# Performance work log

Hardware: AMD Instinct MI355X
Metric: run time of the kernel (lower is better)

The kernel has to match this reference:

```python
import jax, jax.numpy as jnp
import numpy as np

B, N, DIM = 32, 1024, 768
H, S, D = 16, 4, 64  # num_heads, num_subheads (L=H*S=64), attn_dim


def setup_inputs() -> dict:
    key = jax.random.key(0)
    k1, k2, k3, k4 = jax.random.split(key, 4)
    x = jax.random.normal(k1, (B, N, DIM), dtype=jnp.float32)
    eos_indices = jax.random.randint(k2, (B,), 0, N)
    # q_emb: original shape (1,H,S,1,D); singleton dims dropped -> (H,S,D)
    q_emb = jax.random.normal(k3, (H, S, D), dtype=jnp.float32)
    # k Linear(dim -> H*D), xavier-uniform weight, zero bias (share_kv: v == k)
    limit = float(np.sqrt(6.0 / (DIM + H * D)))
    Wk = jax.random.uniform(k4, (DIM, H * D), dtype=jnp.float32, minval=-limit, maxval=limit)
    bk = jnp.zeros((H * D,), dtype=jnp.float32)
    return {"x": x, "eos_indices": eos_indices, "q_emb": q_emb, "Wk": Wk, "bk": bk}


def reference(x, eos_indices, q_emb, Wk, bk):
    # x: (B,N,dim); shared k/v projection -> (B,N,H,D)
    kv = (x @ Wk + bk).reshape(x.shape[0], x.shape[1], H, D)
    scale = D ** -0.5
    # Avoid the torch expand over subheads: contract directly.
    # logits: (B,H,S,N)
    logits = jnp.einsum("hsd,bnhd->bhsn", q_emb * scale, kv)
    # eos masking: positions strictly after eos index are masked out
    mask = jnp.arange(x.shape[1])[None, None, None, :] > eos_indices[:, None, None, None]
    logits = jnp.where(mask, -jnp.inf, logits)
    attn = jax.nn.softmax(logits, axis=-1)
    # weighted sum over N -> (B,H,S,D) -> (B,L,D)
    out = jnp.einsum("bhsn,bnhd->bhsd", attn, kv)
    return out.reshape(x.shape[0], H * S, D)
```

## Files before the change

kernel.cpp:

```cpp
#include <hip/hip_runtime.h>
#include <hip/hip_bf16.h>
#include <stdint.h>

typedef float  f32x4  __attribute__((ext_vector_type(4)));
typedef __bf16 bf16x4 __attribute__((ext_vector_type(4)));
typedef __bf16 bf16x8 __attribute__((ext_vector_type(8)));
typedef unsigned int u32x2 __attribute__((ext_vector_type(2)));
typedef unsigned int u32x4 __attribute__((ext_vector_type(4)));

#define AS1 __attribute__((address_space(1)))
#define AS3 __attribute__((address_space(3)))

__device__ __forceinline__ void async_load16(const void* g, void* lds) {
    __builtin_amdgcn_global_load_lds((const AS1 unsigned int*)g,
                                     (AS3 unsigned int*)lds, 16, 0, 0);
}

__global__ __launch_bounds__(256) void bias_init(const float* __restrict__ bk,
                                                 float* __restrict__ out) {
    const int idx = blockIdx.x * 256 + threadIdx.x;
    out[idx] = bk[((idx >> 8) & 15) * 64 + (idx & 63)];
}

__global__ __launch_bounds__(256) void qw_kernel(const float* __restrict__ q_emb,
                                                 const float* __restrict__ wk,
                                                 __bf16* __restrict__ qwT) {
    __shared__ float qlds[256];
    __shared__ float part[4096];
    const int t = threadIdx.x;
    const int kc = blockIdx.x;
    const int h  = blockIdx.y;
    const int k0 = kc * 64;
    qlds[t] = q_emb[h * 256 + t] * 0.125f;
    __syncthreads();
    const int dseg = t & 15;
    const int krow = t >> 4;
#pragma unroll
    for (int i = 0; i < 4; ++i) {
        const int k = i * 16 + krow;
        f32x4 wv = *(const f32x4*)&wk[(size_t)(k0 + k) * 1024 + h * 64 + dseg * 4];
#pragma unroll
        for (int s = 0; s < 4; ++s) {
            float p = qlds[s * 64 + dseg * 4 + 0] * wv[0]
                    + qlds[s * 64 + dseg * 4 + 1] * wv[1]
                    + qlds[s * 64 + dseg * 4 + 2] * wv[2]
                    + qlds[s * 64 + dseg * 4 + 3] * wv[3];
            part[k * 64 + s * 16 + dseg] = p;
        }
    }
    __syncthreads();
    const int k = t >> 2, s = t & 3;
    const float* pp = &part[k * 64 + s * 16];
    float sum = 0.f;
#pragma unroll
    for (int j = 0; j < 16; ++j) sum += pp[j];
    qwT[(h * 4 + s) * 768 + k0 + k] = (__bf16)sum;
}

__global__ __launch_bounds__(512) void logits_kernel(const float* __restrict__ x,
                                                     const __bf16* __restrict__ qwT,
                                                     const int* __restrict__ eos_idx,
                                                     __bf16* __restrict__ Lg,
                                                     float* __restrict__ partials) {
    __shared__ char smem[49152];
    char* Bl = smem;
    char* Al = smem + 16384;
    const int t = threadIdx.x, l = t & 63, w = t >> 6;
    const int m0 = blockIdx.x * 128;
    const int bb = m0 >> 10, n0 = m0 & 1023;
    const int chunk = blockIdx.x & 7;
    const int wrA = (w >> 1) * 32;
    const int wcB = (w & 1) * 32;

    f32x4 acc[2][2];
#pragma unroll
    for (int i = 0; i < 2; ++i)
#pragma unroll
        for (int j = 0; j < 2; ++j) acc[i][j] = (f32x4)0.f;

    const int Bcol = t >> 3, Bseg = t & 7;
    const __bf16* qsrc = qwT + Bcol * 768 + (Bseg ^ (Bcol & 7)) * 8;
    const int Arow0 = t >> 4;
    const int Aseg = t & 15;

    f32x4 av[4];
    async_load16(qsrc, Bl + t * 16);
#pragma unroll
    for (int i = 0; i < 4; ++i)
        av[i] = *(const f32x4*)&x[(size_t)(m0 + i * 32 + Arow0) * 768 + Aseg * 4];
#pragma unroll
    for (int i = 0; i < 4; ++i) {
        const int row = i * 32 + Arow0;
        bf16x4 vv = {(__bf16)av[i][0], (__bf16)av[i][1], (__bf16)av[i][2], (__bf16)av[i][3]};
        *(bf16x4*)(Al + ((row * 128 + Aseg * 8) ^ ((row & 7) << 4))) = vv;
    }
    asm volatile("s_waitcnt vmcnt(0)" ::: "memory");
    __syncthreads();

    int buf = 0;
    for (int step = 0; step < 12; ++step) {
        const int nbuf = buf ^ 1;
        const bool more = (step + 1) < 12;
        if (more) {
            const int kt = (step + 1) * 64;
            async_load16(qsrc + kt, Bl + nbuf * 8192 + t * 16);
#pragma unroll
            for (int i = 0; i < 4; ++i)
                av[i] = *(const f32x4*)&x[(size_t)(m0 + i * 32 + Arow0) * 768 + kt + Aseg * 4];
        }
#pragma unroll
        for (int kh = 0; kh < 2; ++kh) {
            const int u = kh * 4 + (l >> 4);
            bf16x8 af[2], bfr[2];
#pragma unroll
            for (int i = 0; i < 2; ++i) {
                const int row = wrA + i * 16 + (l & 15);
                af[i] = *(const bf16x8*)(Al + buf * 16384 +
                                         ((row * 128 + u * 16) ^ ((row & 7) << 4)));
            }
#pragma unroll
            for (int j = 0; j < 2; ++j) {
                const int col = wcB + j * 16 + (l & 15);
                bfr[j] = *(const bf16x8*)(Bl + buf * 8192 +
                                          ((col * 128 + u * 16) ^ ((col & 7) << 4)));
            }
#pragma unroll
            for (int i = 0; i < 2; ++i)
#pragma unroll
                for (int j = 0; j < 2; ++j)
                    acc[i][j] = __builtin_amdgcn_mfma_f32_16x16x32_bf16(
                        af[i], bfr[j], acc[i][j], 0, 0, 0);
        }
        if (more) {
#pragma unroll
            for (int i = 0; i < 4; ++i) {
                const int row = i * 32 + Arow0;
                bf16x4 vv = {(__bf16)av[i][0], (__bf16)av[i][1], (__bf16)av[i][2], (__bf16)av[i][3]};
                *(bf16x4*)(Al + nbuf * 16384 + ((row * 128 + Aseg * 8) ^ ((row & 7) << 4))) = vv;
            }
        }
        asm volatile("s_waitcnt vmcnt(0)" ::: "memory");
        __syncthreads();
        buf = nbuf;
    }

#pragma unroll
    for (int i = 0; i < 2; ++i)
#pragma unroll
        for (int j = 0; j < 2; ++j) {
            const int hs = wcB + j * 16 + (l & 15);
            const int nb = wrA + i * 16 + (l >> 4) * 4;
            *(f32x4*)(smem + ((hs * 512 + nb * 4) ^ ((hs & 7) << 4))) = acc[i][j];
        }
    __syncthreads();
    const int eosb = eos_idx[bb];
    const int hs = t >> 3, seg7 = t & 7;
    const int fH = (hs & 7) << 4;
    float mx = -INFINITY;
    bf16x4 pk4[4];
#pragma unroll
    for (int i = 0; i < 4; ++i) {
        const int seg = seg7 + i * 8;
        f32x4 v = *(const f32x4*)(smem + ((hs * 512 + seg * 16) ^ fH));
        bf16x4 pk;
#pragma unroll
        for (int j = 0; j < 4; ++j) {
            const float f = (n0 + seg * 4 + j > eosb) ? -INFINITY : v[j];
            pk[j] = (__bf16)f;
            mx = fmaxf(mx, (float)pk[j]);
        }
        pk4[i] = pk;
        *(bf16x4*)&Lg[(size_t)bb * 65536 + hs * 1024 + n0 + seg * 4] = pk;
    }
#pragma unroll
    for (int off = 1; off < 8; off <<= 1) mx = fmaxf(mx, __shfl_xor(mx, off));
    float sl = 0.f;
    if (mx > -INFINITY) {
#pragma unroll
        for (int i = 0; i < 4; ++i)
#pragma unroll
            for (int j = 0; j < 4; ++j) sl += __expf((float)pk4[i][j] - mx);
    }
#pragma unroll
    for (int off = 1; off < 8; off <<= 1) sl += __shfl_xor(sl, off);
    if (seg7 == 0) {
        float2 st = {mx, sl};
        *(float2*)&partials[(size_t)(((bb * 8 + chunk) * 64) + hs) * 2] = st;
    }
}

__global__ __launch_bounds__(256, 3) void pv_kernel(const float* __restrict__ x,
                                                    const __bf16* __restrict__ Lg,
                                                    const float* __restrict__ partials,
                                                    const float* __restrict__ wk,
                                                    float* __restrict__ out_p) {
    __shared__ char smem[32768];
    char* Pl = smem;
    char* Xl = smem + 16384;
    const int t = threadIdx.x, l = t & 63, w = t >> 6;
    const int vid = (blockIdx.x & 7) * 48 + (blockIdx.x >> 3);
    const int b = vid / 12, kc = vid % 12;
    const int k0 = kc * 64;
    const int wrA = (w >> 1) * 32, wcB = (w & 1) * 32;
    const __bf16* Lgb = Lg + (size_t)b * 65536;
    const float* xb = x + (size_t)b * 786432 + k0 + l;
    const int fK = ((l & 7) << 4) | (((l >> 3) & 1) << 3);

    const int r0 = t >> 3, r1 = 32 + (t >> 3);
    float m0r, i0r, m1r, i1r;
    {
        const float* pb = partials + (size_t)b * 1024;
        float m = -INFINITY, m2 = -INFINITY;
#pragma unroll
        for (int c = 0; c < 8; ++c) {
            m  = fmaxf(m,  pb[(c * 64 + r0) * 2]);
            m2 = fmaxf(m2, pb[(c * 64 + r1) * 2]);
        }
        float s = 0.f, s2 = 0.f;
#pragma unroll
        for (int c = 0; c < 8; ++c) {
            float2 p0 = *(const float2*)&pb[(c * 64 + r0) * 2];
            float2 p1 = *(const float2*)&pb[(c * 64 + r1) * 2];
            s  += p0.y * __expf(p0.x - m);
            s2 += p1.y * __expf(p1.x - m2);
        }
        m0r = m; i0r = 1.0f / s;
        m1r = m2; i1r = 1.0f / s2;
    }
    const int n0s0 = (((t & 7) ^ (r0 & 7)) * 8);
    const int n0s1 = (((t & 7) ^ (r1 & 7)) * 8);

    f32x4 acc[2][2];
#pragma unroll
    for (int i = 0; i < 2; ++i)
#pragma unroll
        for (int j = 0; j < 2; ++j) acc[i][j] = (f32x4)0.f;

    auto STAGE = [&](int bufb, int T) {
        bf16x8 g0 = *(const bf16x8*)&Lgb[(size_t)r0 * 1024 + T * 64 + n0s0];
        bf16x8 g1 = *(const bf16x8*)&Lgb[(size_t)r1 * 1024 + T * 64 + n0s1];
        float xv[16];
#pragma unroll
        for (int i_ = 0; i_ < 4; ++i_)
#pragma unroll
            for (int j_ = 0; j_ < 4; ++j_)
                xv[i_ * 4 + j_] = xb[(size_t)(T * 64 + i_ * 16 + w * 4 + j_) * 768];
        bf16x8 pk;
#pragma unroll
        for (int j_ = 0; j_ < 8; ++j_)
            pk[j_] = (__bf16)(__expf((float)g0[j_] - m0r) * i0r);
        *(bf16x8*)(Pl + bufb * 8192 + t * 16) = pk;
#pragma unroll
        for (int j_ = 0; j_ < 8; ++j_)
            pk[j_] = (__bf16)(__expf((float)g1[j_] - m1r) * i1r);
        *(bf16x8*)(Pl + bufb * 8192 + 4096 + t * 16) = pk;
#pragma unroll
        for (int i_ = 0; i_ < 4; ++i_) {
            bf16x4 vv = {(__bf16)xv[i_ * 4 + 0], (__bf16)xv[i_ * 4 + 1],
                         (__bf16)xv[i_ * 4 + 2], (__bf16)xv[i_ * 4 + 3]};
            *(bf16x4*)(Xl + bufb * 8192 + ((l * 128 + (i_ * 16 + w * 4) * 2) ^ fK)) = vv;
        }
    };
    auto COMPUTE = [&](int bufb) {
#pragma unroll
        for (int kh = 0; kh < 2; ++kh) {
            const int u = kh * 4 + (l >> 4);
            bf16x8 af[2], bfr[2];
#pragma unroll
            for (int i = 0; i < 2; ++i) {
                const int row = wrA + i * 16 + (l & 15);
                af[i] = *(const bf16x8*)(Pl + bufb * 8192 +
                                         ((row * 128 + u * 16) ^ ((row & 7) << 4)));
            }
#pragma unroll
            for (int j = 0; j < 2; ++j) {
                const int kcol = wcB + j * 16 + (l & 15);
                const int fKc = ((kcol & 7) << 4) | (((kcol >> 3) & 1) << 3);
                const int addrA = kcol * 128 + kh * 64 + (l >> 4) * 16;
                u32x2 lo = *(const u32x2*)(Xl + bufb * 8192 + (addrA ^ fKc));
                u32x2 hi = *(const u32x2*)(Xl + bufb * 8192 + ((addrA + 8) ^ fKc));
                u32x4 uu = {lo[0], lo[1], hi[0], hi[1]};
                bfr[j] = __builtin_bit_cast(bf16x8, uu);
            }
#pragma unroll
            for (int i = 0; i < 2; ++i)
#pragma unroll
                for (int j = 0; j < 2; ++j)
                    acc[i][j] = __builtin_amdgcn_mfma_f32_16x16x32_bf16(
                        af[i], bfr[j], acc[i][j], 0, 0, 0);
        }
    };

    STAGE(0, 0);
    __syncthreads();
    int buf = 0;
    for (int step = 0; step < 16; ++step) {
        if (step + 1 < 16) STAGE(buf ^ 1, step + 1);
        COMPUTE(buf);
        __syncthreads();
        buf ^= 1;
    }

#pragma unroll
    for (int i = 0; i < 2; ++i)
#pragma unroll
        for (int j = 0; j < 2; ++j) {
            const int kcol = wcB + j * 16 + (l & 15);
#pragma unroll
            for (int r = 0; r < 4; ++r) {
                const int hs2 = wrA + i * 16 + (l >> 4) * 4 + r;
                *(float*)(smem + ((hs2 * 256 + kcol * 4) ^ ((hs2 & 7) << 4))) = acc[i][j][r];
            }
        }
    __syncthreads();

    const int d = l;
#pragma unroll
    for (int hh = 0; hh < 4; ++hh) {
        const int h = w * 4 + hh;
        const float* wcol = &wk[(size_t)k0 * 1024 + h * 64 + d];
        float ao0 = 0.f, ao1 = 0.f, ao2 = 0.f, ao3 = 0.f;
#pragma unroll 4
        for (int kq = 0; kq < 16; ++kq) {
            const float wv0 = wcol[(size_t)(kq * 4 + 0) * 1024];
            const float wv1 = wcol[(size_t)(kq * 4 + 1) * 1024];
            const float wv2 = wcol[(size_t)(kq * 4 + 2) * 1024];
            const float wv3 = wcol[(size_t)(kq * 4 + 3) * 1024];
            const int hsb = h * 4;
            f32x4 y0 = *(const f32x4*)(smem + (((hsb + 0) * 256 + kq * 16) ^ (((hsb + 0) & 7) << 4)));
            f32x4 y1 = *(const f32x4*)(smem + (((hsb + 1) * 256 + kq * 16) ^ (((hsb + 1) & 7) << 4)));
            f32x4 y2 = *(const f32x4*)(smem + (((hsb + 2) * 256 + kq * 16) ^ (((hsb + 2) & 7) << 4)));
            f32x4 y3 = *(const f32x4*)(smem + (((hsb + 3) * 256 + kq * 16) ^ (((hsb + 3) & 7) << 4)));
            ao0 += y0[0] * wv0 + y0[1] * wv1 + y0[2] * wv2 + y0[3] * wv3;
            ao1 += y1[0] * wv0 + y1[1] * wv1 + y1[2] * wv2 + y1[3] * wv3;
            ao2 += y2[0] * wv0 + y2[1] * wv1 + y2[2] * wv2 + y2[3] * wv3;
            ao3 += y3[0] * wv0 + y3[1] * wv1 + y3[2] * wv2 + y3[3] * wv3;
        }
        float* ob = &out_p[(size_t)(b * 64 + h * 4) * 64 + d];
        atomicAdd(ob +   0, ao0);
        atomicAdd(ob +  64, ao1);
        atomicAdd(ob + 128, ao2);
        atomicAdd(ob + 192, ao3);
    }
}

extern "C" void kernel_launch(void* const* d_in, const int* in_sizes, int n_in,
                              void* d_out, int out_size, void* d_ws, size_t ws_size,
                              hipStream_t stream) {
    const float* x     = (const float*)d_in[0];
    const int*   eos   = (const int*)d_in[1];
    const float* q_emb = (const float*)d_in[2];
    const float* Wk    = (const float*)d_in[3];
    const float* bk    = (const float*)d_in[4];
    float* out = (float*)d_out;

    char* ws = (char*)d_ws;
    __bf16* qwT      = (__bf16*)ws;
    __bf16* Lg       = (__bf16*)(ws + 131072);
    float*  partials = (float*)(ws + 131072 + 4194304);

    bias_init<<<dim3(512), 256, 0, stream>>>(bk, out);
    qw_kernel<<<dim3(12, 16), 256, 0, stream>>>(q_emb, Wk, qwT);
    logits_kernel<<<dim3(256), 512, 0, stream>>>(x, qwT, eos, Lg, partials);
    pv_kernel<<<dim3(384), 256, 0, stream>>>(x, Lg, partials, Wk, out);
}
```

Baseline: 66.30 us.

## Split output projection into separate kernel, drop bias init and atomics

```diff
diff --git a/kernel.cpp b/kernel.cpp
--- a/kernel.cpp
+++ b/kernel.cpp
@@ -14,12 +14,6 @@
 __device__ __forceinline__ void async_load16(const void* g, void* lds) {
     __builtin_amdgcn_global_load_lds((const AS1 unsigned int*)g,
                                      (AS3 unsigned int*)lds, 16, 0, 0);
-}
-
-__global__ __launch_bounds__(256) void bias_init(const float* __restrict__ bk,
-                                                 float* __restrict__ out) {
-    const int idx = blockIdx.x * 256 + threadIdx.x;
-    out[idx] = bk[((idx >> 8) & 15) * 64 + (idx & 63)];
 }
 
 __global__ __launch_bounds__(256) void qw_kernel(const float* __restrict__ q_emb,
@@ -192,8 +186,7 @@
 __global__ __launch_bounds__(256, 3) void pv_kernel(const float* __restrict__ x,
                                                     const __bf16* __restrict__ Lg,
                                                     const float* __restrict__ partials,
-                                                    const float* __restrict__ wk,
-                                                    float* __restrict__ out_p) {
+                                                    float* __restrict__ y) {
     __shared__ char smem[32768];
     char* Pl = smem;
     char* Xl = smem + 16384;
@@ -313,34 +306,58 @@
             }
         }
     __syncthreads();
-
-    const int d = l;
-#pragma unroll
-    for (int hh = 0; hh < 4; ++hh) {
-        const int h = w * 4 + hh;
-        const float* wcol = &wk[(size_t)k0 * 1024 + h * 64 + d];
-        float ao0 = 0.f, ao1 = 0.f, ao2 = 0.f, ao3 = 0.f;
-#pragma unroll 4
-        for (int kq = 0; kq < 16; ++kq) {
-            const float wv0 = wcol[(size_t)(kq * 4 + 0) * 1024];
-            const float wv1 = wcol[(size_t)(kq * 4 + 1) * 1024];
-            const float wv2 = wcol[(size_t)(kq * 4 + 2) * 1024];
-            const float wv3 = wcol[(size_t)(kq * 4 + 3) * 1024];
-            const int hsb = h * 4;
-            f32x4 y0 = *(const f32x4*)(smem + (((hsb + 0) * 256 + kq * 16) ^ (((hsb + 0) & 7) << 4)));
-            f32x4 y1 = *(const f32x4*)(smem + (((hsb + 1) * 256 + kq * 16) ^ (((hsb + 1) & 7) << 4)));
-            f32x4 y2 = *(const f32x4*)(smem + (((hsb + 2) * 256 + kq * 16) ^ (((hsb + 2) & 7) << 4)));
-            f32x4 y3 = *(const f32x4*)(smem + (((hsb + 3) * 256 + kq * 16) ^ (((hsb + 3) & 7) << 4)));
-            ao0 += y0[0] * wv0 + y0[1] * wv1 + y0[2] * wv2 + y0[3] * wv3;
-            ao1 += y1[0] * wv0 + y1[1] * wv1 + y1[2] * wv2 + y1[3] * wv3;
-            ao2 += y2[0] * wv0 + y2[1] * wv1 + y2[2] * wv2 + y2[3] * wv3;
-            ao3 += y3[0] * wv0 + y3[1] * wv1 + y3[2] * wv2 + y3[3] * wv3;
-        }
-        float* ob = &out_p[(size_t)(b * 64 + h * 4) * 64 + d];
-        atomicAdd(ob +   0, ao0);
-        atomicAdd(ob +  64, ao1);
-        atomicAdd(ob + 128, ao2);
-        atomicAdd(ob + 192, ao3);
+    const int hs2 = t >> 2;
+#pragma unroll
+    for (int i = 0; i < 4; ++i) {
+        const int seg = (t & 3) + i * 4;
+        f32x4 v = *(const f32x4*)(smem + ((hs2 * 256 + seg * 16) ^ ((hs2 & 7) << 4)));
+        *(f32x4*)&y[(size_t)(b * 64 + hs2) * 768 + k0 + seg * 4] = v;
+    }
+}
+
+__global__ __launch_bounds__(256) void out_kernel(const float* __restrict__ y,
+                                                  const float* __restrict__ wk,
+                                                  const float* __restrict__ bk,
+                                                  float* __restrict__ out) {
+    __shared__ float ylds[8 * 768];
+    __shared__ float red[2048];
+    const int t = threadIdx.x;
+    const int vid = (blockIdx.x & 7) * 32 + (blockIdx.x >> 3);
+    const int h = vid >> 4, bp = vid & 15;
+#pragma unroll
+    for (int r = 0; r < 8; ++r) {
+        const int gb = bp * 2 + (r >> 2);
+        const int hs = h * 4 + (r & 3);
+#pragma unroll
+        for (int i = 0; i < 3; ++i)
+            ylds[r * 768 + i * 256 + t] = y[(size_t)(gb * 64 + hs) * 768 + i * 256 + t];
+    }
+    __syncthreads();
+    const int kp = t >> 6, d = t & 63;
+    float acc[8] = {0.f, 0.f, 0.f, 0.f, 0.f, 0.f, 0.f, 0.f};
+    for (int i = 0; i < 48; ++i) {
+        const int k = kp * 192 + i * 4;
+        const float wv0 = wk[(size_t)(k + 0) * 1024 + h * 64 + d];
+        const float wv1 = wk[(size_t)(k + 1) * 1024 + h * 64 + d];
+        const float wv2 = wk[(size_t)(k + 2) * 1024 + h * 64 + d];
+        const float wv3 = wk[(size_t)(k + 3) * 1024 + h * 64 + d];
+#pragma unroll
+        for (int r = 0; r < 8; ++r) {
+            f32x4 yv = *(const f32x4*)&ylds[r * 768 + k];
+            acc[r] += yv[0] * wv0 + yv[1] * wv1 + yv[2] * wv2 + yv[3] * wv3;
+        }
+    }
+#pragma unroll
+    for (int r = 0; r < 8; ++r) red[(r * 64 + d) * 4 + kp] = acc[r];
+    __syncthreads();
+#pragma unroll
+    for (int i = 0; i < 2; ++i) {
+        const int o = i * 256 + t;
+        const int r = o >> 6, dd = o & 63;
+        f32x4 pv = *(const f32x4*)&red[o * 4];
+        const float s = pv[0] + pv[1] + pv[2] + pv[3] + bk[h * 64 + dd];
+        const int gb = bp * 2 + (r >> 2);
+        out[(size_t)(gb * 64 + h * 4 + (r & 3)) * 64 + dd] = s;
     }
 }
 
@@ -357,10 +374,11 @@
     char* ws = (char*)d_ws;
     __bf16* qwT      = (__bf16*)ws;
     __bf16* Lg       = (__bf16*)(ws + 131072);
-    float*  partials = (float*)(ws + 131072 + 4194304);
-
-    bias_init<<<dim3(512), 256, 0, stream>>>(bk, out);
+    float*  partials = (float*)(ws + 4325376);
+    float*  y        = (float*)(ws + 4456448);
+
     qw_kernel<<<dim3(12, 16), 256, 0, stream>>>(q_emb, Wk, qwT);
     logits_kernel<<<dim3(256), 512, 0, stream>>>(x, qwT, eos, Lg, partials);
-    pv_kernel<<<dim3(384), 256, 0, stream>>>(x, Lg, partials, Wk, out);
-}
+    pv_kernel<<<dim3(384), 256, 0, stream>>>(x, Lg, partials, y);
+    out_kernel<<<dim3(256), 256, 0, stream>>>(y, Wk, bk, out);
+}
```

Result: faster. 63.76 us (-3.8%).
